# Kernel optimization log

Hardware: AMD Instinct MI355X
Metric: run time of the kernel (lower is better)

Reference implementation:

```python
import jax, jax.numpy as jnp
import numpy as np

N_NODES = 50000
N_EDGES = 625000
IN_CH = 128
OUT_CH = 128


def setup_inputs() -> dict:
    key = jax.random.key(0)
    k1, k2, k3, k4 = jax.random.split(key, 4)
    x = jax.random.normal(k1, (N_NODES, IN_CH), dtype=jnp.float32)
    edge_index = jax.random.randint(k2, (2, N_EDGES), 0, N_NODES, dtype=jnp.int64)
    # nn.Linear(in, out): weight [out, in], bias [out]
    bound = 1.0 / np.sqrt(IN_CH)
    W = jax.random.uniform(k3, (OUT_CH, IN_CH), minval=-bound, maxval=bound, dtype=jnp.float32)
    b = jax.random.uniform(k4, (OUT_CH,), minval=-bound, maxval=bound, dtype=jnp.float32)
    return {"x": x, "edge_index": edge_index, "W": W, "b": b}


def reference(x, edge_index, W, b):
    row, col = edge_index[0], edge_index[1]
    num_nodes = x.shape[0]
    # degree of destination nodes (scatter_add of ones over row)
    deg = jax.ops.segment_sum(jnp.ones(row.shape[0], dtype=x.dtype), row,
                              num_segments=num_nodes)
    deg_inv_sqrt = jnp.where(deg > 0, jax.lax.rsqrt(jnp.maximum(deg, 1.0)) * jnp.where(deg > 0, 1.0, 0.0), 0.0)
    deg_inv_sqrt = jnp.where(deg > 0, deg ** -0.5, 0.0)
    norm = deg_inv_sqrt[row] * deg_inv_sqrt[col]  # [E]
    src = x[col] * norm[:, None]                  # gather + scale, [E, C]
    out = jax.ops.segment_sum(src, row, num_segments=num_nodes)  # scatter-add
    return out @ W.T + b
```

## Files before the change

kernel.cpp:

```cpp
#include <hip/hip_runtime.h>
#include <hip/hip_bf16.h>

#define NN 50000
#define NE 625000
#define CH 128
#define RSTR 32
#define NG 196
#define GCAP 4096
#define NBIN 256
#define EPB 2442

typedef __attribute__((ext_vector_type(8))) short short8;
typedef __attribute__((ext_vector_type(4))) float floatx4;

__device__ __forceinline__ ushort f2bf(float v) {
    __hip_bfloat16 h = __float2bfloat16(v);
    return *(ushort*)&h;
}
__device__ __forceinline__ float bf2f(uint u) {
    return __uint_as_float(u << 16);
}

__global__ __launch_bounds__(256) void k_prep(const float* __restrict__ x,
                                              ushort* __restrict__ xb,
                                              const float* __restrict__ W,
                                              ushort* __restrict__ whi,
                                              ushort* __restrict__ wlo,
                                              const int* __restrict__ row,
                                              const int* __restrict__ col,
                                              uint* __restrict__ gbase,
                                              uint* __restrict__ gseg) {
    __shared__ uint h[NG];
    __shared__ uint sc[NG];
    __shared__ uint gb[NG];
    __shared__ uint cur[NG];
    __shared__ uint ss[256];
    __shared__ uint pk[EPB];

    int b = blockIdx.x;
    int t = threadIdx.x;
    if (b < NBIN) {
        int e0 = b * EPB;
        int n = NE - e0; if (n > EPB) n = EPB;

        for (int i = t; i < NG; i += 256) h[i] = 0;
        __syncthreads();

        int r[10], c[10];
#pragma unroll
        for (int j = 0; j < 10; ++j) {
            int i = t + j * 256;
            int idx = (i < n) ? (e0 + i) : e0;
            r[j] = row[idx];
            c[j] = col[idx];
        }
#pragma unroll
        for (int j = 0; j < 10; ++j)
            if (t + j * 256 < n) atomicAdd(&h[r[j] >> 8], 1u);
        __syncthreads();

        ss[t] = (t < NG) ? h[t] : 0u;
        __syncthreads();
        for (int off = 1; off < 256; off <<= 1) {
            uint add = (t >= off) ? ss[t - off] : 0u;
            __syncthreads();
            ss[t] += add;
            __syncthreads();
        }
        if (t < NG) {
            uint ex = (t == 0) ? 0u : ss[t - 1];
            sc[t] = ex;
            cur[t] = ex;
            if (h[t] > 0) gb[t] = atomicAdd(&gbase[t], h[t]);
        }
        __syncthreads();

#pragma unroll
        for (int j = 0; j < 10; ++j) {
            if (t + j * 256 < n) {
                int g = r[j] >> 8;
                uint p = atomicAdd(&cur[g], 1u);
                pk[p] = ((uint)(r[j] & 255) << 16) | (uint)(c[j] & 0xffff);
            }
        }
        __syncthreads();

        for (int i = t; i < n; i += 256) {
            int lo = 0, hi = NG - 1;
            while (lo < hi) {
                int mid = (lo + hi + 1) >> 1;
                if (sc[mid] <= (uint)i) lo = mid; else hi = mid - 1;
            }
            int g = lo;
            uint off = gb[g] + ((uint)i - sc[g]);
            if (off < GCAP) gseg[(size_t)g * GCAP + off] = pk[i];
        }
    } else if (b < 6506) {
        int i = ((b - 256) * 256 + t) * 4;
        float4 v = *(const float4*)(x + i);
        ushort4 o;
        o.x = f2bf(v.x); o.y = f2bf(v.y); o.z = f2bf(v.z); o.w = f2bf(v.w);
        *(ushort4*)(xb + i) = o;
    } else {
        int i = (b - 6506) * 256 + t;
        float v = W[i];
        ushort hh = f2bf(v);
        whi[i] = hh;
        wlo[i] = f2bf(v - bf2f((uint)hh));
    }
}

__global__ __launch_bounds__(256) void k_csr(const uint* __restrict__ gseg,
                                             const uint* __restrict__ gcnt,
                                             uint* __restrict__ csr,
                                             int* __restrict__ deg_c,
                                             float* __restrict__ nrm) {
    __shared__ ushort slots[64][62];
    __shared__ uint dcnt[64];
    int g = blockIdx.x >> 2;
    int q = blockIdx.x & 3;
    int t = threadIdx.x;

    int n = (int)gcnt[g];
    if (n > GCAP) n = GCAP;
    if (t < 64) dcnt[t] = 0;
    __syncthreads();

    const uint* seg = gseg + (size_t)g * GCAP;
    for (int i = t; i < n; i += 256) {
        uint p = seg[i];
        int rl = (int)(p >> 16);
        if ((rl >> 6) == q) {
            int r6 = rl & 63;
            uint k = atomicAdd(&dcnt[r6], 1u);
            if (k < 62) slots[r6][k] = (ushort)(p & 0xffff);
        }
    }
    __syncthreads();

    int row0 = g * 256 + q * 64;
    for (int i = t; i < 2048; i += 256) {
        int rl = i >> 5, w = i & 31;
        int rr = row0 + rl;
        if (rr < NN) {
            uint val;
            if (w == 0) val = dcnt[rl];
            else val = (uint)slots[rl][2 * w - 2] | ((uint)slots[rl][2 * w - 1] << 16);
            csr[(size_t)rr * RSTR + w] = val;
        }
    }
    if (t < 64) {
        int rr = row0 + t;
        if (rr < NN) {
            int d = (int)dcnt[t];
            deg_c[rr] = d;
            nrm[rr] = (d > 0) ? rsqrtf((float)d) : 0.0f;
        }
    }
}

__global__ __launch_bounds__(256) void k_aggm(const ushort* __restrict__ xb,
                                              const int* __restrict__ deg_c,
                                              const float* __restrict__ nrm,
                                              const uint* __restrict__ csr,
                                              const ushort* __restrict__ whi,
                                              const ushort* __restrict__ wlo,
                                              const float* __restrict__ bias,
                                              float* __restrict__ out) {
    __shared__ ushort at[32 * 128];
    const int wave = threadIdx.x >> 6;
    const int lane = threadIdx.x & 63;
    const int half = lane >> 5;
    const int lq = lane & 31;
    const int m0 = blockIdx.x * 32;
    const int li = (lane < 62) ? lane : 0;

    int node0 = m0 + wave * 8;
    int deg_n = 0; ushort craw_n = 0; float dr_n = 0.0f;
    if (node0 < NN) {
        deg_n  = deg_c[node0];
        craw_n = ((const ushort*)(csr + (size_t)node0 * RSTR))[2 + li];
        dr_n   = nrm[node0];
    }
    for (int s = 0; s < 8; ++s) {
        int node = node0 + s;
        int r = wave * 8 + s;
        if (node >= NN) {
            if (half == 0) {
                int byte = (r * 256 + lq * 8) ^ ((r & 7) << 4);
                *(uint2*)((char*)at + byte) = make_uint2(0u, 0u);
            }
            continue;
        }
        int deg = deg_n; ushort craw = craw_n; float dr = dr_n;
        int cli = (lane < deg) ? (int)craw : 0;
        float nl = (lane < deg) ? nrm[cli] : 0.0f;
        int nxt = node + 1;
        if (s < 7 && nxt < NN) {
            deg_n  = deg_c[nxt];
            craw_n = ((const ushort*)(csr + (size_t)nxt * RSTR))[2 + li];
            dr_n   = nrm[nxt];
        }
        float a0 = 0.f, a1 = 0.f, a2 = 0.f, a3 = 0.f;
        for (int j = 0; j < deg; j += 8) {
#pragma unroll
            for (int up = 0; up < 4; ++up) {
                int i0 = j + 2 * up;
                int   c0 = __builtin_amdgcn_readlane(cli, i0);
                int   c1 = __builtin_amdgcn_readlane(cli, i0 + 1);
                float n0 = __uint_as_float(__builtin_amdgcn_readlane(__float_as_uint(nl), i0));
                float n1 = __uint_as_float(__builtin_amdgcn_readlane(__float_as_uint(nl), i0 + 1));
                int   cc = half ? c1 : c0;
                float nw = half ? n1 : n0;
                uint2 v = *(const uint2*)(xb + (size_t)cc * CH + lq * 4);
                a0 = fmaf(__uint_as_float(v.x << 16),          nw, a0);
                a1 = fmaf(__uint_as_float(v.x & 0xffff0000u),  nw, a1);
                a2 = fmaf(__uint_as_float(v.y << 16),          nw, a2);
                a3 = fmaf(__uint_as_float(v.y & 0xffff0000u),  nw, a3);
            }
        }
        a0 += __shfl_xor(a0, 32);
        a1 += __shfl_xor(a1, 32);
        a2 += __shfl_xor(a2, 32);
        a3 += __shfl_xor(a3, 32);
        if (half == 0) {
            uint w0 = (uint)f2bf(a0 * dr) | ((uint)f2bf(a1 * dr) << 16);
            uint w1 = (uint)f2bf(a2 * dr) | ((uint)f2bf(a3 * dr) << 16);
            int byte = (r * 256 + lq * 8) ^ ((r & 7) << 4);
            *(uint2*)((char*)at + byte) = make_uint2(w0, w1);
        }
    }
    __syncthreads();

    const int quad = lane >> 4;
    const int r16 = lane & 15;
    const int nt0 = wave * 2, nt1 = nt0 + 1;
    const ushort* bh0p = whi + (size_t)(nt0 * 16 + r16) * CH + quad * 8;
    const ushort* bl0p = wlo + (size_t)(nt0 * 16 + r16) * CH + quad * 8;
    const ushort* bh1p = whi + (size_t)(nt1 * 16 + r16) * CH + quad * 8;
    const ushort* bl1p = wlo + (size_t)(nt1 * 16 + r16) * CH + quad * 8;

    float b0 = bias[nt0 * 16 + r16];
    float b1 = bias[nt1 * 16 + r16];
    floatx4 acc00 = {b0, b0, b0, b0};
    floatx4 acc01 = {b1, b1, b1, b1};
    floatx4 acc10 = {b0, b0, b0, b0};
    floatx4 acc11 = {b1, b1, b1, b1};

    const int swz = (r16 & 7) << 4;
#pragma unroll
    for (int kb = 0; kb < 4; ++kb) {
        const int cb = quad * 16 + kb * 64;
        short8 A0 = *(const short8*)((const char*)at + ((r16 * 256 + cb) ^ swz));
        short8 A1 = *(const short8*)((const char*)at + (((r16 + 16) * 256 + cb) ^ swz));
        const int k0 = kb * 32;
        short8 h0 = *(const short8*)(bh0p + k0);
        short8 l0 = *(const short8*)(bl0p + k0);
        short8 h1 = *(const short8*)(bh1p + k0);
        short8 l1 = *(const short8*)(bl1p + k0);
        acc00 = __builtin_amdgcn_mfma_f32_16x16x32_bf16(A0, h0, acc00, 0, 0, 0);
        acc00 = __builtin_amdgcn_mfma_f32_16x16x32_bf16(A0, l0, acc00, 0, 0, 0);
        acc01 = __builtin_amdgcn_mfma_f32_16x16x32_bf16(A0, h1, acc01, 0, 0, 0);
        acc01 = __builtin_amdgcn_mfma_f32_16x16x32_bf16(A0, l1, acc01, 0, 0, 0);
        acc10 = __builtin_amdgcn_mfma_f32_16x16x32_bf16(A1, h0, acc10, 0, 0, 0);
        acc10 = __builtin_amdgcn_mfma_f32_16x16x32_bf16(A1, l0, acc10, 0, 0, 0);
        acc11 = __builtin_amdgcn_mfma_f32_16x16x32_bf16(A1, h1, acc11, 0, 0, 0);
        acc11 = __builtin_amdgcn_mfma_f32_16x16x32_bf16(A1, l1, acc11, 0, 0, 0);
    }

#pragma unroll
    for (int r = 0; r < 4; ++r) {
        int row0 = m0 + quad * 4 + r;
        int row1 = row0 + 16;
        if (row0 < NN) {
            out[(size_t)row0 * CH + nt0 * 16 + r16] = acc00[r];
            out[(size_t)row0 * CH + nt1 * 16 + r16] = acc01[r];
        }
        if (row1 < NN) {
            out[(size_t)row1 * CH + nt0 * 16 + r16] = acc10[r];
            out[(size_t)row1 * CH + nt1 * 16 + r16] = acc11[r];
        }
    }
}

extern "C" void kernel_launch(void* const* d_in, const int* in_sizes, int n_in,
                              void* d_out, int out_size, void* d_ws, size_t ws_size,
                              hipStream_t stream) {
    const float* x = (const float*)d_in[0];
    const int* ei = (const int*)d_in[1];
    const float* W = (const float*)d_in[2];
    const float* b = (const float*)d_in[3];
    float* out = (float*)d_out;

    uint* csr = (uint*)d_ws;
    int* deg_c = (int*)(csr + (size_t)NN * RSTR);
    float* nrm = (float*)(deg_c + 50176);
    ushort* ahi = (ushort*)(nrm + 50176);
    ushort* xb = ahi + (size_t)(NN + 16) * CH;
    ushort* whi = xb + (size_t)NN * CH;
    ushort* wlo = whi + CH * CH;
    uint* gbase = (uint*)(wlo + CH * CH);
    uint* gseg = gbase + 256;

    hipMemsetAsync(gbase, 0, NG * sizeof(uint), stream);
    k_prep<<<6570, 256, 0, stream>>>(x, xb, W, whi, wlo, ei, ei + NE, gbase, gseg);
    k_csr<<<NG * 4, 256, 0, stream>>>(gseg, gbase, csr, deg_c, nrm);
    k_aggm<<<(NN + 31) / 32, 256, 0, stream>>>(xb, deg_c, nrm, csr, whi, wlo, b, out);
}
```

Baseline: 141.1 us.

## Replace global atomic bucketing with per-block run table for CSR build

```diff
diff --git a/kernel.cpp b/kernel.cpp
--- a/kernel.cpp
+++ b/kernel.cpp
@@ -6,9 +6,8 @@
 #define CH 128
 #define RSTR 32
 #define NG 196
-#define GCAP 4096
-#define NBIN 256
-#define EPB 2442
+#define NBIN 512
+#define EPB 1221
 
 typedef __attribute__((ext_vector_type(8))) short short8;
 typedef __attribute__((ext_vector_type(4))) float floatx4;
@@ -28,12 +27,10 @@
                                               ushort* __restrict__ wlo,
                                               const int* __restrict__ row,
                                               const int* __restrict__ col,
-                                              uint* __restrict__ gbase,
+                                              uint* __restrict__ runtbl,
                                               uint* __restrict__ gseg) {
-    __shared__ uint h[NG];
+    __shared__ uint cnt[NG];
     __shared__ uint sc[NG];
-    __shared__ uint gb[NG];
-    __shared__ uint cur[NG];
     __shared__ uint ss[256];
     __shared__ uint pk[EPB];
 
@@ -43,23 +40,26 @@
         int e0 = b * EPB;
         int n = NE - e0; if (n > EPB) n = EPB;
 
-        for (int i = t; i < NG; i += 256) h[i] = 0;
-        __syncthreads();
-
-        int r[10], c[10];
-#pragma unroll
-        for (int j = 0; j < 10; ++j) {
+        for (int i = t; i < NG; i += 256) cnt[i] = 0;
+        __syncthreads();
+
+        int r[5], c[5], g[5];
+        uint rk[5];
+#pragma unroll
+        for (int j = 0; j < 5; ++j) {
             int i = t + j * 256;
             int idx = (i < n) ? (e0 + i) : e0;
             r[j] = row[idx];
             c[j] = col[idx];
         }
 #pragma unroll
-        for (int j = 0; j < 10; ++j)
-            if (t + j * 256 < n) atomicAdd(&h[r[j] >> 8], 1u);
-        __syncthreads();
-
-        ss[t] = (t < NG) ? h[t] : 0u;
+        for (int j = 0; j < 5; ++j) {
+            g[j] = r[j] >> 8;
+            if (t + j * 256 < n) rk[j] = atomicAdd(&cnt[g[j]], 1u);
+        }
+        __syncthreads();
+
+        ss[t] = (t < NG) ? cnt[t] : 0u;
         __syncthreads();
         for (int off = 1; off < 256; off <<= 1) {
             uint add = (t >= off) ? ss[t - off] : 0u;
@@ -68,41 +68,30 @@
             __syncthreads();
         }
         if (t < NG) {
-            uint ex = (t == 0) ? 0u : ss[t - 1];
-            sc[t] = ex;
-            cur[t] = ex;
-            if (h[t] > 0) gb[t] = atomicAdd(&gbase[t], h[t]);
-        }
-        __syncthreads();
-
-#pragma unroll
-        for (int j = 0; j < 10; ++j) {
+            sc[t] = ss[t] - cnt[t];
+            runtbl[(size_t)t * NBIN + b] = (sc[t] << 12) | cnt[t];
+        }
+        __syncthreads();
+
+#pragma unroll
+        for (int j = 0; j < 5; ++j) {
             if (t + j * 256 < n) {
-                int g = r[j] >> 8;
-                uint p = atomicAdd(&cur[g], 1u);
-                pk[p] = ((uint)(r[j] & 255) << 16) | (uint)(c[j] & 0xffff);
+                uint pos = sc[g[j]] + rk[j];
+                pk[pos] = ((uint)(r[j] & 255) << 16) | (uint)(c[j] & 0xffff);
             }
         }
         __syncthreads();
 
-        for (int i = t; i < n; i += 256) {
-            int lo = 0, hi = NG - 1;
-            while (lo < hi) {
-                int mid = (lo + hi + 1) >> 1;
-                if (sc[mid] <= (uint)i) lo = mid; else hi = mid - 1;
-            }
-            int g = lo;
-            uint off = gb[g] + ((uint)i - sc[g]);
-            if (off < GCAP) gseg[(size_t)g * GCAP + off] = pk[i];
-        }
-    } else if (b < 6506) {
-        int i = ((b - 256) * 256 + t) * 4;
+        for (int i = t; i < n; i += 256)
+            gseg[e0 + i] = pk[i];
+    } else if (b < 6762) {
+        int i = ((b - 512) * 256 + t) * 4;
         float4 v = *(const float4*)(x + i);
         ushort4 o;
         o.x = f2bf(v.x); o.y = f2bf(v.y); o.z = f2bf(v.z); o.w = f2bf(v.w);
         *(ushort4*)(xb + i) = o;
     } else {
-        int i = (b - 6506) * 256 + t;
+        int i = (b - 6762) * 256 + t;
         float v = W[i];
         ushort hh = f2bf(v);
         whi[i] = hh;
@@ -111,29 +100,36 @@
 }
 
 __global__ __launch_bounds__(256) void k_csr(const uint* __restrict__ gseg,
-                                             const uint* __restrict__ gcnt,
+                                             const uint* __restrict__ runtbl,
                                              uint* __restrict__ csr,
                                              int* __restrict__ deg_c,
                                              float* __restrict__ nrm) {
     __shared__ ushort slots[64][62];
     __shared__ uint dcnt[64];
+    __shared__ uint rt[NBIN];
     int g = blockIdx.x >> 2;
     int q = blockIdx.x & 3;
     int t = threadIdx.x;
 
-    int n = (int)gcnt[g];
-    if (n > GCAP) n = GCAP;
     if (t < 64) dcnt[t] = 0;
+    for (int i = t; i < NBIN; i += 256)
+        rt[i] = runtbl[(size_t)g * NBIN + i];
     __syncthreads();
 
-    const uint* seg = gseg + (size_t)g * GCAP;
-    for (int i = t; i < n; i += 256) {
-        uint p = seg[i];
-        int rl = (int)(p >> 16);
-        if ((rl >> 6) == q) {
-            int r6 = rl & 63;
-            uint k = atomicAdd(&dcnt[r6], 1u);
-            if (k < 62) slots[r6][k] = (ushort)(p & 0xffff);
+#pragma unroll
+    for (int rep = 0; rep < NBIN / 256; ++rep) {
+        int bb = t + rep * 256;
+        uint d = rt[bb];
+        uint s = d >> 12, len = d & 0xFFFu;
+        const uint* p = gseg + (size_t)bb * EPB + s;
+        for (uint k = 0; k < len; ++k) {
+            uint e = p[k];
+            int rl = (int)(e >> 16);
+            if ((rl >> 6) == q) {
+                int r6 = rl & 63;
+                uint kk = atomicAdd(&dcnt[r6], 1u);
+                if (kk < 62) slots[r6][kk] = (ushort)(e & 0xffff);
+            }
         }
     }
     __syncthreads();
@@ -299,11 +295,10 @@
     ushort* xb = ahi + (size_t)(NN + 16) * CH;
     ushort* whi = xb + (size_t)NN * CH;
     ushort* wlo = whi + CH * CH;
-    uint* gbase = (uint*)(wlo + CH * CH);
-    uint* gseg = gbase + 256;
-
-    hipMemsetAsync(gbase, 0, NG * sizeof(uint), stream);
-    k_prep<<<6570, 256, 0, stream>>>(x, xb, W, whi, wlo, ei, ei + NE, gbase, gseg);
-    k_csr<<<NG * 4, 256, 0, stream>>>(gseg, gbase, csr, deg_c, nrm);
+    uint* runtbl = (uint*)(wlo + CH * CH);
+    uint* gseg = runtbl + (size_t)NG * NBIN;
+
+    k_prep<<<6826, 256, 0, stream>>>(x, xb, W, whi, wlo, ei, ei + NE, runtbl, gseg);
+    k_csr<<<784, 256, 0, stream>>>(gseg, runtbl, csr, deg_c, nrm);
     k_aggm<<<(NN + 31) / 32, 256, 0, stream>>>(xb, deg_c, nrm, csr, whi, wlo, b, out);
 }
```

After: 137.6 us. -2.5%, faster.
